# Performance work log

Hardware: AMD Instinct MI355X
Metric: run time of the kernel (lower is better)

The kernel has to match this reference:

```python
import jax, jax.numpy as jnp
import numpy as np

B, S, D = 8, 512, 768      # batch, seq_len, hidden_size (BERT-base)
E, F = 4, 3072             # num_experts, intermediate (4*D)


def setup_inputs() -> dict:
    key = jax.random.key(0)
    ks = jax.random.split(key, 8)
    x = jax.random.normal(ks[0], (B, S, D), dtype=jnp.float32)
    input_ids = jax.random.randint(ks[1], (B, S), 0, 30522, dtype=jnp.int64)
    attention_mask = jnp.ones((B, S), dtype=jnp.float32)
    # gate: nn.Linear(hidden_size, num_experts, bias=False) -> weight [E, D]
    gate_w = jax.random.normal(ks[2], (E, D), dtype=jnp.float32) * 0.02
    # experts: BERT FFN  Linear(D,F) + GELU + Linear(F,D), stacked over experts
    W1 = jax.random.normal(ks[3], (E, D, F), dtype=jnp.float32) * 0.02
    b1 = jnp.zeros((E, F), dtype=jnp.float32)
    W2 = jax.random.normal(ks[4], (E, F, D), dtype=jnp.float32) * 0.02
    b2 = jnp.zeros((E, D), dtype=jnp.float32)
    return {"x": x, "input_ids": input_ids, "attention_mask": attention_mask,
            "gate_w": gate_w, "W1": W1, "b1": b1, "W2": W2, "b2": b2}


def reference(x, input_ids, attention_mask, gate_w, W1, b1, W2, b2):
    # route_method == 'gate-token' (training path, straight-through combine)
    b, s, d = x.shape
    e = gate_w.shape[0]
    xf = x.reshape(-1, d)                                   # [N, D]
    logits = xf @ gate_w.T                                  # [N, E]
    prob = jax.nn.softmax(logits, axis=-1)                  # [N, E]
    gate = jnp.argmax(prob, axis=-1)                        # [N]
    sel = jax.nn.one_hot(gate, e, dtype=xf.dtype)           # [N, E]
    gate_load = jnp.sum(sel, axis=0).astype(jnp.int32)      # tokens per expert
    # load-balancing loss:  E * sum(mean(prob) * fraction_of_tokens)
    P = prob.mean(axis=0)
    f = gate_load.astype(xf.dtype) / jnp.sum(gate_load).astype(xf.dtype)
    balance_loss = e * jnp.sum(P * f)
    # prob of the chosen expert per token
    p = jnp.take_along_axis(prob, gate[:, None], axis=1)    # [N, 1]
    # all-expert FFN (the torch code runs every expert on every token group)
    h = jax.nn.gelu(jnp.einsum('nd,edf->enf', xf, W1) + b1[:, None, :],
                    approximate=False)                      # [E, N, F]
    outs = jnp.einsum('enf,efd->end', h, W2) + b2[:, None, :]  # [E, N, D]
    # straight-through coefficients: selected -> 1 - sg(p) + p, others -> p - sg(p)
    st = p - jax.lax.stop_gradient(p)                       # [N, 1] (==0 in value)
    coef = sel.T[:, :, None] + st[None, :, :]               # [E, N, 1]
    out = jnp.sum(outs * coef, axis=0).reshape(b, s, d)
    return out, balance_loss, gate_load
```

## Files before the change

### kernel.cpp

```cpp
#include <hip/hip_runtime.h>
#include <hip/hip_bf16.h>
#include <stdint.h>
#include <math.h>

#define NTOK 4096
#define DIM 768
#define FF 3072
#define NE 4
#define MAXGT 40

typedef __attribute__((ext_vector_type(8))) short bf16x8;
typedef __attribute__((ext_vector_type(4))) float f32x4;
typedef unsigned short u16;

static __device__ __forceinline__ u16 f2bf(float f) {
    union { float f; unsigned u; } c; c.f = f;
    unsigned r = (c.u + 0x7FFFu + ((c.u >> 16) & 1u)) >> 16;
    return (u16)r;
}

static __device__ __forceinline__ float fast_erff(float x) {
    float ax = fabsf(x);
    float t = 1.0f / (1.0f + 0.3275911f * ax);
    float p = ((((1.061405429f * t - 1.453152027f) * t) + 1.421413741f) * t
               - 0.284496736f) * t + 0.254829592f;
    float y = 1.0f - p * t * __expf(-ax * ax);
    return copysignf(y, x);
}

#define GLD_LDS16(g, l) __builtin_amdgcn_global_load_lds( \
    (const __attribute__((address_space(1))) void*)(g),   \
    (__attribute__((address_space(3))) void*)(l), 16, 0, 0)


static __device__ __forceinline__ void transpose_tile(
    const float* __restrict__ src, u16* __restrict__ dst, float* tile,
    int cx, int ry, int Ccols, int NSs, int CTs, int e)
{
    const int r0 = ry * 64, c0 = cx * 64;
    #pragma unroll
    for (int p = 0; p < 4; ++p) {
        int f = p * 256 + threadIdx.x;
        int row = f >> 4, c4 = (f & 15) * 4;
        float4 v = *(const float4*)(src + (size_t)(r0 + row) * Ccols + c0 + c4);
        tile[row * 65 + c4 + 0] = v.x;
        tile[row * 65 + c4 + 1] = v.y;
        tile[row * 65 + c4 + 2] = v.z;
        tile[row * 65 + c4 + 3] = v.w;
    }
    __syncthreads();
    #pragma unroll
    for (int p = 0; p < 2; ++p) {
        int u = p * 256 + threadIdx.x;
        int orow = u >> 3, g = (u & 7) * 8;
        bf16x8 v;
        #pragma unroll
        for (int j = 0; j < 8; ++j)
            v[j] = (short)f2bf(tile[(g + j) * 65 + orow]);
        const int n = c0 + orow;
        const int ct = n >> 7, rr = n & 127;
        const int k = r0 + g;
        const int t = k >> 5, c = (k >> 3) & 3;
        const int unit = ((rr * 4 + c) ^ (rr & 7));
        *(bf16x8*)(dst + ((size_t)((e * CTs + ct) * NSs + t) << 12) + unit * 8) = v;
    }
}

__global__ __launch_bounds__(256) void w1gate_kernel(
    const float* __restrict__ W1, const float* __restrict__ x,
    const float* __restrict__ gw, u16* __restrict__ W1tp,
    float* __restrict__ probs, int* __restrict__ eid, u16* __restrict__ xbf)
{
    __shared__ float tile[64 * 65];
    if (blockIdx.x < 2304) {
        const int b2 = blockIdx.x;
        const int e = b2 / 576, rem = b2 % 576;
        transpose_tile(W1 + (size_t)e * DIM * FF, W1tp, tile,
                       rem % 48, rem / 48, FF, DIM / 32, FF / 128, e);
        return;
    }
    const int wid = threadIdx.x >> 6, lane = threadIdx.x & 63;
    const int n = (blockIdx.x - 2304) * 4 + wid;
    const float4* xr4 = (const float4*)(x + (size_t)n * DIM);
    float a0 = 0.f, a1 = 0.f, a2 = 0.f, a3 = 0.f;
    float4 xv[3];
    #pragma unroll
    for (int c = 0; c < 3; c++) {
        float4 v = xr4[c * 64 + lane];
        xv[c] = v;
        const float4 g0 = ((const float4*)(gw + 0 * DIM))[c * 64 + lane];
        const float4 g1 = ((const float4*)(gw + 1 * DIM))[c * 64 + lane];
        const float4 g2 = ((const float4*)(gw + 2 * DIM))[c * 64 + lane];
        const float4 g3 = ((const float4*)(gw + 3 * DIM))[c * 64 + lane];
        a0 += v.x * g0.x + v.y * g0.y + v.z * g0.z + v.w * g0.w;
        a1 += v.x * g1.x + v.y * g1.y + v.z * g1.z + v.w * g1.w;
        a2 += v.x * g2.x + v.y * g2.y + v.z * g2.z + v.w * g2.w;
        a3 += v.x * g3.x + v.y * g3.y + v.z * g3.z + v.w * g3.w;
    }
    #pragma unroll
    for (int c = 0; c < 3; c++) {
        ushort4 o;
        o.x = f2bf(xv[c].x); o.y = f2bf(xv[c].y);
        o.z = f2bf(xv[c].z); o.w = f2bf(xv[c].w);
        *(ushort4*)(xbf + (size_t)n * DIM + (c * 64 + lane) * 4) = o;
    }
    #pragma unroll
    for (int off = 32; off > 0; off >>= 1) {
        a0 += __shfl_xor(a0, off);
        a1 += __shfl_xor(a1, off);
        a2 += __shfl_xor(a2, off);
        a3 += __shfl_xor(a3, off);
    }
    if (lane == 0) {
        float l[4] = {a0, a1, a2, a3};
        float m = fmaxf(fmaxf(l[0], l[1]), fmaxf(l[2], l[3]));
        float p[4], s = 0.f;
        #pragma unroll
        for (int e = 0; e < 4; e++) { p[e] = expf(l[e] - m); s += p[e]; }
        float inv = 1.f / s;
        int amax = 0; float best = l[0];
        #pragma unroll
        for (int e = 1; e < 4; e++) if (l[e] > best) { best = l[e]; amax = e; }
        #pragma unroll
        for (int e = 0; e < 4; e++) probs[n * 4 + e] = p[e] * inv;
        eid[n] = amax;
    }
}

__global__ __launch_bounds__(256) void w2scan_kernel(
    const float* __restrict__ W2, u16* __restrict__ W2tp,
    const int4* __restrict__ eid4, const float4* __restrict__ probs4,
    int* __restrict__ counts, int* __restrict__ tlist, float* __restrict__ tail)
{
    __shared__ __align__(16) char smem[64 * 65 * 4];
    if (blockIdx.x < 2304) {
        const int b2 = blockIdx.x;
        const int e = b2 / 576, rem = b2 % 576;
        transpose_tile(W2 + (size_t)e * DIM * FF, W2tp, (float*)smem,
                       rem % 12, rem / 12, DIM, FF / 32, DIM / 128, e);
        return;
    }
    int4* scA = (int4*)smem;
    int4* scB = scA + 256;
    float4* sp = (float4*)(scB + 256);
    const int t = threadIdx.x;
    int es[16];
    int c[4] = {0, 0, 0, 0};
    #pragma unroll
    for (int i = 0; i < 4; i++) {
        int4 e4 = eid4[t * 4 + i];
        es[i * 4 + 0] = e4.x; es[i * 4 + 1] = e4.y;
        es[i * 4 + 2] = e4.z; es[i * 4 + 3] = e4.w;
    }
    #pragma unroll
    for (int i = 0; i < 16; i++) c[es[i]]++;
    scA[t] = make_int4(c[0], c[1], c[2], c[3]);
    float4 ps = make_float4(0.f, 0.f, 0.f, 0.f);
    #pragma unroll
    for (int i = 0; i < 16; i++) {
        float4 v = probs4[t * 16 + i];
        ps.x += v.x; ps.y += v.y; ps.z += v.z; ps.w += v.w;
    }
    sp[t] = ps;
    __syncthreads();
    int4 *cur = scA, *nxt = scB;
    for (int off = 1; off < 256; off <<= 1) {
        int4 v = cur[t];
        if (t >= off) {
            int4 u = cur[t - off];
            v.x += u.x; v.y += u.y; v.z += u.z; v.w += u.w;
        }
        nxt[t] = v;
        int4* tmp = cur; cur = nxt; nxt = tmp;
        __syncthreads();
    }
    const int4 incl = cur[t];
    const int4 tot4 = cur[255];
    int base[4] = {incl.x - c[0], incl.y - c[1], incl.z - c[2], incl.w - c[3]};
    int run[4] = {0, 0, 0, 0};
    #pragma unroll
    for (int i = 0; i < 16; i++) {
        const int e = es[i];
        tlist[e * NTOK + base[e] + run[e]] = t * 16 + i;
        run[e]++;
    }
    for (int s = 128; s > 0; s >>= 1) {
        if (t < s) {
            float4 a = sp[t], b = sp[t + s];
            a.x += b.x; a.y += b.y; a.z += b.z; a.w += b.w;
            sp[t] = a;
        }
        __syncthreads();
    }
    if (t == 0) {
        int tot[4] = {tot4.x, tot4.y, tot4.z, tot4.w};
        float Ps[4] = {sp[0].x, sp[0].y, sp[0].z, sp[0].w};
        int tb = 0;
        counts[8] = 0;
        float bl = 0.f;
        #pragma unroll
        for (int e = 0; e < 4; e++) {
            counts[e] = tot[e];
            bl += (Ps[e] / (float)NTOK) * ((float)tot[e] / (float)NTOK);
            tb += (tot[e] + 127) >> 7;
            counts[9 + e] = tb;
        }
        tail[0] = bl * (float)NE;
        #pragma unroll
        for (int e = 0; e < 4; e++) tail[1 + e] = (float)tot[e];
    }
}

__global__ __launch_bounds__(256) void packA_kernel(
    const u16* __restrict__ xbf, const int* __restrict__ counts,
    const int* __restrict__ tlist, u16* __restrict__ Apack)
{
    const int gt = blockIdx.x >> 3, pp = blockIdx.x & 7;
    const int* tb = counts + 8;
    if (gt >= tb[4]) return;
    const int e = (gt >= tb[1]) + (gt >= tb[2]) + (gt >= tb[3]);
    const int rt = gt - tb[e];
    const int cnt = counts[e];
    for (int u = pp * 1536 + threadIdx.x; u < (pp + 1) * 1536; u += 256) {
        const int t = u >> 9, j = u & 511;
        const int r = ((j >> 3) << 1) | (((j >> 2) & 1) ^ ((j >> 4) & 1));
        const int c = (j & 3) ^ (r & 3);
        const int pos = rt * 128 + r;
        const int tok = tlist[e * NTOK + min(pos, cnt - 1)];
        *(bf16x8*)(Apack + ((size_t)(gt * (DIM / 32) + t) << 12) + j * 8) =
            *(const bf16x8*)(xbf + (size_t)tok * DIM + t * 32 + c * 8);
    }
}

template <int KD, int NCOL, int GELU>
__global__ __launch_bounds__(512, 2) void moe_gemm(
    const u16* __restrict__ Apk, const u16* __restrict__ Bpk,
    const float* __restrict__ bias, const int* __restrict__ counts,
    const int* __restrict__ tlist, u16* __restrict__ OutP,
    float* __restrict__ OutF)
{
    constexpr int NS = KD / 64;
    constexpr int KC = KD / 32;
    constexpr int CT = NCOL / 128;

    const int gt = blockIdx.x / CT;
    const int ct = blockIdx.x % CT;
    const int* tb = counts + 8;
    if (gt >= tb[4]) return;
    const int e = (gt >= tb[1]) + (gt >= tb[2]) + (gt >= tb[3]);
    const int rt = gt - tb[e];
    const int cnt = counts[e];

    __shared__ __align__(16) u16 L[2][2][2][4096];

    const int tid = threadIdx.x, lane = tid & 63, w = tid >> 6;
    const u16* mats[2] = {
        Apk + ((size_t)(gt * KC) << 12),
        Bpk + ((size_t)((e * CT + ct) * KC) << 12)};

    const int wm = w >> 2, wn = w & 3;
    const int fr = lane & 15, fg = lane >> 4;
    const int laneoff = (fr * 64 + fg * 16) ^ ((fr & 7) << 4);

    f32x4 acc[4][2];
    #pragma unroll
    for (int i = 0; i < 4; i++)
        #pragma unroll
        for (int j = 0; j < 2; j++) acc[i][j] = (f32x4){0.f, 0.f, 0.f, 0.f};

    auto stage = [&](int T) {
        const int b = T & 1;
        #pragma unroll
        for (int l = 0; l < 4; ++l) {
            const int s = w * 4 + l;
            const int mat = s >> 4, sub = s & 15, kc = sub >> 3, u8 = sub & 7;
            GLD_LDS16(mats[mat] + ((size_t)(2 * T + kc) << 12) + u8 * 512,
                      &L[b][mat][kc][u8 * 512]);
        }
    };
    auto compute = [&](int T) {
        const int b = T & 1;
        #pragma unroll
        for (int ks = 0; ks < 2; ++ks) {
            const char* LA = (const char*)&L[b][0][ks][0];
            const char* LB = (const char*)&L[b][1][ks][0];
            bf16x8 bg[2];
            #pragma unroll
            for (int n = 0; n < 2; ++n)
                bg[n] = *(const bf16x8*)(LB + (wn * 2 + n) * 1024 + laneoff);
            #pragma unroll
            for (int m = 0; m < 4; ++m) {
                bf16x8 af = *(const bf16x8*)(LA + (wm * 4 + m) * 1024 + laneoff);
                #pragma unroll
                for (int n = 0; n < 2; ++n)
                    acc[m][n] = __builtin_amdgcn_mfma_f32_16x16x32_bf16(
                        af, bg[n], acc[m][n], 0, 0, 0);
            }
        }
    };

    stage(0); stage(1);
    for (int t = 0; t < NS; ++t) {
        if (t < NS - 1)
            asm volatile("s_waitcnt vmcnt(4)" ::: "memory");
        else
            asm volatile("s_waitcnt vmcnt(0)" ::: "memory");
        __builtin_amdgcn_sched_barrier(0);
        __builtin_amdgcn_s_barrier();
        __builtin_amdgcn_sched_barrier(0);
        compute(t);
        __builtin_amdgcn_sched_barrier(0);
        __builtin_amdgcn_s_barrier();
        __builtin_amdgcn_sched_barrier(0);
        if (t + 2 < NS) stage(t + 2);
    }

    #pragma unroll
    for (int m = 0; m < 4; ++m) {
        #pragma unroll
        for (int r2 = 0; r2 < 4; r2++) {
            const int row = wm * 64 + m * 16 + fg * 4 + r2;
            #pragma unroll
            for (int n = 0; n < 2; ++n) {
                const int col = ct * 128 + wn * 32 + n * 16 + fr;
                float v = acc[m][n][r2] + bias[e * NCOL + col];
                if (GELU) {
                    v = 0.5f * v * (1.f + fast_erff(v * 0.70710678118654752f));
                    const int unit = ((row * 4 + ((col >> 3) & 3)) ^ (row & 7));
                    OutP[((size_t)(gt * (NCOL / 32) + (col >> 5)) << 12) + unit * 8 +
                         (col & 7)] = f2bf(v);
                } else {
                    const int pos = rt * 128 + row;
                    if (pos < cnt) {
                        const int tok = tlist[e * NTOK + pos];
                        OutF[(size_t)tok * NCOL + col] = v;
                    }
                }
            }
        }
    }
}

extern "C" void kernel_launch(void* const* d_in, const int* in_sizes, int n_in,
                              void* d_out, int out_size, void* d_ws, size_t ws_size,
                              hipStream_t stream) {
    const float* x  = (const float*)d_in[0];
    const float* gw = (const float*)d_in[3];
    const float* W1 = (const float*)d_in[4];
    const float* b1 = (const float*)d_in[5];
    const float* W2 = (const float*)d_in[6];
    const float* b2 = (const float*)d_in[7];
    float* out = (float*)d_out;

    char* ws = (char*)d_ws;
    size_t o = 0;
    auto alloc = [&](size_t bytes) -> void* {
        void* p = ws + o;
        o = (o + bytes + 255) & ~(size_t)255;
        return p;
    };
    u16*   xbf    = (u16*)alloc((size_t)NTOK * DIM * 2);
    u16*   Apack  = (u16*)alloc((size_t)MAXGT * 128 * DIM * 2);
    u16*   W1tp   = (u16*)alloc((size_t)NE * DIM * FF * 2);
    u16*   W2tp   = (u16*)alloc((size_t)NE * DIM * FF * 2);
    u16*   hbuf   = (u16*)alloc((size_t)MAXGT * 128 * FF * 2);
    float* probs  = (float*)alloc((size_t)NTOK * 4 * 4);
    int*   tlist  = (int*)alloc((size_t)NE * NTOK * 4);
    int*   eid    = (int*)alloc((size_t)NTOK * 4);
    int*   counts = (int*)alloc(256);

    w1gate_kernel<<<2304 + 1024, 256, 0, stream>>>(
        W1, x, gw, W1tp, probs, eid, xbf);
    w2scan_kernel<<<2305, 256, 0, stream>>>(
        W2, W2tp, (const int4*)eid, (const float4*)probs, counts, tlist,
        out + (size_t)NTOK * DIM);
    packA_kernel<<<MAXGT * 8, 256, 0, stream>>>(xbf, counts, tlist, Apack);

    moe_gemm<DIM, FF, 1><<<MAXGT * (FF / 128), 512, 0, stream>>>(
        Apack, W1tp, b1, counts, tlist, hbuf, nullptr);
    moe_gemm<FF, DIM, 0><<<MAXGT * (DIM / 128), 512, 0, stream>>>(
        hbuf, W2tp, b2, counts, tlist, nullptr, out);
}
```

Before: 105.4 us.

## Move W2 transpose into GEMM1 launch to overlap with compute

The W2 fp32-to-bf16 transpose/pack moves out of the scan kernel and into extra blocks of the first expert GEMM launch. Each 512-thread block does two 64x64 tiles, one per half-block, reusing the GEMM's LDS. The scan now runs as a single-block kernel. The aim is to hide the W2 conversion's memory traffic behind the compute-bound GEMM1 and shorten the serial scan step. The risk is that the transpose blocks compete with GEMM blocks for CUs and bandwidth, and that the GEMM's launch bounds may restrict their occupancy.

```diff
diff --git a/kernel.cpp b/kernel.cpp
--- a/kernel.cpp
+++ b/kernel.cpp
@@ -34,13 +34,13 @@
 
 
 static __device__ __forceinline__ void transpose_tile(
-    const float* __restrict__ src, u16* __restrict__ dst, float* tile,
+    const float* __restrict__ src, u16* __restrict__ dst, float* tile, int tid,
     int cx, int ry, int Ccols, int NSs, int CTs, int e)
 {
     const int r0 = ry * 64, c0 = cx * 64;
     #pragma unroll
     for (int p = 0; p < 4; ++p) {
-        int f = p * 256 + threadIdx.x;
+        int f = p * 256 + tid;
         int row = f >> 4, c4 = (f & 15) * 4;
         float4 v = *(const float4*)(src + (size_t)(r0 + row) * Ccols + c0 + c4);
         tile[row * 65 + c4 + 0] = v.x;
@@ -51,7 +51,7 @@
     __syncthreads();
     #pragma unroll
     for (int p = 0; p < 2; ++p) {
-        int u = p * 256 + threadIdx.x;
+        int u = p * 256 + tid;
         int orow = u >> 3, g = (u & 7) * 8;
         bf16x8 v;
         #pragma unroll
@@ -75,7 +75,7 @@
     if (blockIdx.x < 2304) {
         const int b2 = blockIdx.x;
         const int e = b2 / 576, rem = b2 % 576;
-        transpose_tile(W1 + (size_t)e * DIM * FF, W1tp, tile,
+        transpose_tile(W1 + (size_t)e * DIM * FF, W1tp, tile, threadIdx.x,
                        rem % 48, rem / 48, FF, DIM / 32, FF / 128, e);
         return;
     }
@@ -127,22 +127,12 @@
     }
 }
 
-__global__ __launch_bounds__(256) void w2scan_kernel(
-    const float* __restrict__ W2, u16* __restrict__ W2tp,
+__global__ __launch_bounds__(256) void scan_kernel(
     const int4* __restrict__ eid4, const float4* __restrict__ probs4,
     int* __restrict__ counts, int* __restrict__ tlist, float* __restrict__ tail)
 {
-    __shared__ __align__(16) char smem[64 * 65 * 4];
-    if (blockIdx.x < 2304) {
-        const int b2 = blockIdx.x;
-        const int e = b2 / 576, rem = b2 % 576;
-        transpose_tile(W2 + (size_t)e * DIM * FF, W2tp, (float*)smem,
-                       rem % 12, rem / 12, DIM, FF / 32, DIM / 128, e);
-        return;
-    }
-    int4* scA = (int4*)smem;
-    int4* scB = scA + 256;
-    float4* sp = (float4*)(scB + 256);
+    __shared__ int4 scA[256], scB[256];
+    __shared__ float4 sp[256];
     const int t = threadIdx.x;
     int es[16];
     int c[4] = {0, 0, 0, 0};
@@ -232,26 +222,33 @@
     }
 }
 
-template <int KD, int NCOL, int GELU>
-__global__ __launch_bounds__(512, 2) void moe_gemm(
+__global__ __launch_bounds__(512, 2) void gemm1_w2t_kernel(
     const u16* __restrict__ Apk, const u16* __restrict__ Bpk,
     const float* __restrict__ bias, const int* __restrict__ counts,
-    const int* __restrict__ tlist, u16* __restrict__ OutP,
-    float* __restrict__ OutF)
-{
-    constexpr int NS = KD / 64;
-    constexpr int KC = KD / 32;
-    constexpr int CT = NCOL / 128;
+    u16* __restrict__ OutP, const float* __restrict__ W2, u16* __restrict__ W2tp)
+{
+    constexpr int NS = DIM / 64;
+    constexpr int KC = DIM / 32;
+    constexpr int CT = FF / 128;
+
+    __shared__ __align__(16) u16 L[2][2][2][4096];
+
+    if (blockIdx.x >= 960) {
+        const int half = (threadIdx.x >= 256);
+        const int tid = threadIdx.x & 255;
+        const int b2 = (blockIdx.x - 960) * 2 + half;
+        const int e = b2 / 576, rem = b2 % 576;
+        float* tile = (float*)&L[0][0][0][0] + half * (64 * 65);
+        transpose_tile(W2 + (size_t)e * DIM * FF, W2tp, tile, tid,
+                       rem % 12, rem / 12, DIM, FF / 32, DIM / 128, e);
+        return;
+    }
 
     const int gt = blockIdx.x / CT;
     const int ct = blockIdx.x % CT;
     const int* tb = counts + 8;
     if (gt >= tb[4]) return;
     const int e = (gt >= tb[1]) + (gt >= tb[2]) + (gt >= tb[3]);
-    const int rt = gt - tb[e];
-    const int cnt = counts[e];
-
-    __shared__ __align__(16) u16 L[2][2][2][4096];
 
     const int tid = threadIdx.x, lane = tid & 63, w = tid >> 6;
     const u16* mats[2] = {
@@ -323,18 +320,110 @@
             #pragma unroll
             for (int n = 0; n < 2; ++n) {
                 const int col = ct * 128 + wn * 32 + n * 16 + fr;
-                float v = acc[m][n][r2] + bias[e * NCOL + col];
-                if (GELU) {
-                    v = 0.5f * v * (1.f + fast_erff(v * 0.70710678118654752f));
-                    const int unit = ((row * 4 + ((col >> 3) & 3)) ^ (row & 7));
-                    OutP[((size_t)(gt * (NCOL / 32) + (col >> 5)) << 12) + unit * 8 +
-                         (col & 7)] = f2bf(v);
-                } else {
-                    const int pos = rt * 128 + row;
-                    if (pos < cnt) {
-                        const int tok = tlist[e * NTOK + pos];
-                        OutF[(size_t)tok * NCOL + col] = v;
-                    }
+                float v = acc[m][n][r2] + bias[e * FF + col];
+                v = 0.5f * v * (1.f + fast_erff(v * 0.70710678118654752f));
+                const int unit = ((row * 4 + ((col >> 3) & 3)) ^ (row & 7));
+                OutP[((size_t)(gt * (FF / 32) + (col >> 5)) << 12) + unit * 8 +
+                     (col & 7)] = f2bf(v);
+            }
+        }
+    }
+}
+
+__global__ __launch_bounds__(512, 2) void gemm2_kernel(
+    const u16* __restrict__ Apk, const u16* __restrict__ Bpk,
+    const float* __restrict__ bias, const int* __restrict__ counts,
+    const int* __restrict__ tlist, float* __restrict__ out)
+{
+    constexpr int NS = FF / 64;
+    constexpr int KC = FF / 32;
+    constexpr int CT = DIM / 128;
+
+    const int gt = blockIdx.x / CT;
+    const int ct = blockIdx.x % CT;
+    const int* tb = counts + 8;
+    if (gt >= tb[4]) return;
+    const int e = (gt >= tb[1]) + (gt >= tb[2]) + (gt >= tb[3]);
+    const int rt = gt - tb[e];
+    const int cnt = counts[e];
+
+    __shared__ __align__(16) u16 L[2][2][2][4096];
+
+    const int tid = threadIdx.x, lane = tid & 63, w = tid >> 6;
+    const u16* mats[2] = {
+        Apk + ((size_t)(gt * KC) << 12),
+        Bpk + ((size_t)((e * CT + ct) * KC) << 12)};
+
+    const int wm = w >> 2, wn = w & 3;
+    const int fr = lane & 15, fg = lane >> 4;
+    const int laneoff = (fr * 64 + fg * 16) ^ ((fr & 7) << 4);
+
+    f32x4 acc[4][2];
+    #pragma unroll
+    for (int i = 0; i < 4; i++)
+        #pragma unroll
+        for (int j = 0; j < 2; j++) acc[i][j] = (f32x4){0.f, 0.f, 0.f, 0.f};
+
+    auto stage = [&](int T) {
+        const int b = T & 1;
+        #pragma unroll
+        for (int l = 0; l < 4; ++l) {
+            const int s = w * 4 + l;
+            const int mat = s >> 4, sub = s & 15, kc = sub >> 3, u8 = sub & 7;
+            GLD_LDS16(mats[mat] + ((size_t)(2 * T + kc) << 12) + u8 * 512,
+                      &L[b][mat][kc][u8 * 512]);
+        }
+    };
+    auto compute = [&](int T) {
+        const int b = T & 1;
+        #pragma unroll
+        for (int ks = 0; ks < 2; ++ks) {
+            const char* LA = (const char*)&L[b][0][ks][0];
+            const char* LB = (const char*)&L[b][1][ks][0];
+            bf16x8 bg[2];
+            #pragma unroll
+            for (int n = 0; n < 2; ++n)
+                bg[n] = *(const bf16x8*)(LB + (wn * 2 + n) * 1024 + laneoff);
+            #pragma unroll
+            for (int m = 0; m < 4; ++m) {
+                bf16x8 af = *(const bf16x8*)(LA + (wm * 4 + m) * 1024 + laneoff);
+                #pragma unroll
+                for (int n = 0; n < 2; ++n)
+                    acc[m][n] = __builtin_amdgcn_mfma_f32_16x16x32_bf16(
+                        af, bg[n], acc[m][n], 0, 0, 0);
+            }
+        }
+    };
+
+    stage(0); stage(1);
+    for (int t = 0; t < NS; ++t) {
+        if (t < NS - 1)
+            asm volatile("s_waitcnt vmcnt(4)" ::: "memory");
+        else
+            asm volatile("s_waitcnt vmcnt(0)" ::: "memory");
+        __builtin_amdgcn_sched_barrier(0);
+        __builtin_amdgcn_s_barrier();
+        __builtin_amdgcn_sched_barrier(0);
+        compute(t);
+        __builtin_amdgcn_sched_barrier(0);
+        __builtin_amdgcn_s_barrier();
+        __builtin_amdgcn_sched_barrier(0);
+        if (t + 2 < NS) stage(t + 2);
+    }
+
+    #pragma unroll
+    for (int m = 0; m < 4; ++m) {
+        #pragma unroll
+        for (int r2 = 0; r2 < 4; r2++) {
+            const int row = wm * 64 + m * 16 + fg * 4 + r2;
+            const int pos = rt * 128 + row;
+            if (pos < cnt) {
+                const int tok = tlist[e * NTOK + pos];
+                #pragma unroll
+                for (int n = 0; n < 2; ++n) {
+                    const int col = ct * 128 + wn * 32 + n * 16 + fr;
+                    out[(size_t)tok * DIM + col] =
+                        acc[m][n][r2] + bias[e * DIM + col];
                 }
             }
         }
@@ -371,13 +460,13 @@
 
     w1gate_kernel<<<2304 + 1024, 256, 0, stream>>>(
         W1, x, gw, W1tp, probs, eid, xbf);
-    w2scan_kernel<<<2305, 256, 0, stream>>>(
-        W2, W2tp, (const int4*)eid, (const float4*)probs, counts, tlist,
+    scan_kernel<<<1, 256, 0, stream>>>(
+        (const int4*)eid, (const float4*)probs, counts, tlist,
         out + (size_t)NTOK * DIM);
     packA_kernel<<<MAXGT * 8, 256, 0, stream>>>(xbf, counts, tlist, Apack);
 
-    moe_gemm<DIM, FF, 1><<<MAXGT * (FF / 128), 512, 0, stream>>>(
-        Apack, W1tp, b1, counts, tlist, hbuf, nullptr);
-    moe_gemm<FF, DIM, 0><<<MAXGT * (DIM / 128), 512, 0, stream>>>(
-        hbuf, W2tp, b2, counts, tlist, nullptr, out);
-}
+    gemm1_w2t_kernel<<<960 + 1152, 512, 0, stream>>>(
+        Apack, W1tp, b1, counts, hbuf, W2, W2tp);
+    gemm2_kernel<<<MAXGT * (DIM / 128), 512, 0, stream>>>(
+        hbuf, W2tp, b2, counts, tlist, out);
+}
```

New measurement: 99.12 us. 1.06x faster.
